# Kernel optimization log

Measured on AMD Instinct MI355X. Metric: run time of the kernel, lower is better.

Reference implementation:

```python
import jax, jax.numpy as jnp
import numpy as np

N, E, G = 100000, 1600000, 256      # nodes, edges, graphs in batch
IN_C, HID, OUT_C = 4, 128, 120
ALPHA = 0.5


def setup_inputs() -> dict:
    key = jax.random.key(0)
    ks = jax.random.split(key, 12)
    def w(k, i, o):
        return jax.random.normal(k, (i, o), jnp.float32) / np.float32(np.sqrt(i))
    return {
        "x": jax.random.normal(ks[0], (N, IN_C), jnp.float32),
        "edge_index": jax.random.randint(ks[1], (2, E), 0, N),
        "batch_seg": jnp.sort(jax.random.randint(ks[2], (N,), 0, G)),
        # DirGNNConv holds two independent GCNConvs (in / reversed direction)
        "W_in": w(ks[3], IN_C, HID),  "b_in": jnp.zeros((HID,), jnp.float32),
        "W_in_r": w(ks[4], IN_C, HID), "b_in_r": jnp.zeros((HID,), jnp.float32),
        "W_mid": w(ks[5], HID, HID),  "b_mid": jnp.zeros((HID,), jnp.float32),
        "W_mid_r": w(ks[6], HID, HID), "b_mid_r": jnp.zeros((HID,), jnp.float32),
        "W_out": w(ks[7], HID, OUT_C), "b_out": jnp.zeros((OUT_C,), jnp.float32),
        "W_out_r": w(ks[8], HID, OUT_C), "b_out_r": jnp.zeros((OUT_C,), jnp.float32),
    }


def _gcn(x, W, b, src, dst, n):
    # GCNConv with add_self_loops=False (DirGNNConv disables self-loops):
    # deg computed on destination side, norm = deg^-1/2[src] * deg^-1/2[dst]
    deg = jax.ops.segment_sum(jnp.ones(src.shape[0], x.dtype), dst, num_segments=n)
    dinv = jnp.where(deg > 0, jax.lax.rsqrt(jnp.maximum(deg, 1e-12)), 0.0)
    h = x @ W                                  # [N, out]
    msg = h[src] * (dinv[src] * dinv[dst])[:, None]  # gather + edge-normalize
    return jax.ops.segment_sum(msg, dst, num_segments=n) + b


def _dir_conv(x, Wi, bi, Wr, br, src, dst):
    # DirGNNConv(root_weight=False): (1-a)*conv(edge_index) + a*conv(flipped)
    n = x.shape[0]
    x_in = _gcn(x, Wi, bi, src, dst, n)
    x_out = _gcn(x, Wr, br, dst, src, n)
    return ALPHA * x_out + (1.0 - ALPHA) * x_in


def reference(x, edge_index, batch_seg, W_in, b_in, W_in_r, b_in_r,
              W_mid, b_mid, W_mid_r, b_mid_r, W_out, b_out, W_out_r, b_out_r):
    src, dst = edge_index[0], edge_index[1]
    h = jax.nn.relu(_dir_conv(x, W_in, b_in, W_in_r, b_in_r, src, dst))
    # dropout: eval mode -> identity
    h = jax.nn.relu(_dir_conv(h, W_mid, b_mid, W_mid_r, b_mid_r, src, dst))
    h = _dir_conv(h, W_out, b_out, W_out_r, b_out_r, src, dst)
    # global_mean_pool over batch_seg
    sums = jax.ops.segment_sum(h, batch_seg, num_segments=G)
    cnt = jax.ops.segment_sum(jnp.ones((h.shape[0],), h.dtype), batch_seg, num_segments=G)
    return sums / jnp.maximum(cnt, 1.0)[:, None]
```

## Files before the change

### kernel.cpp

```cpp
#include <hip/hip_runtime.h>
#include <hip/hip_fp16.h>

#define ALPHA 0.5f
#define SCAN_B 256
#define BSH 9
#define BSZ 512
#define MAXB 512
#define CHUNK 4096

static inline int ceil_div(int a, int b) { return (a + b - 1) / b; }

struct alignas(8) half4 { __half2 a, b; };

typedef _Float16 half8 __attribute__((ext_vector_type(8)));
typedef float f32x4 __attribute__((ext_vector_type(4)));

__global__ void hist_kernel(const int* __restrict__ src, const int* __restrict__ dst,
                            unsigned int* __restrict__ bhI, unsigned int* __restrict__ bhO,
                            int E, int nbuck)
{
    __shared__ unsigned int hI[MAXB], hO[MAXB];
    for (int b = threadIdx.x; b < MAXB; b += blockDim.x) { hI[b] = 0; hO[b] = 0; }
    __syncthreads();
    for (int e = blockIdx.x * blockDim.x + threadIdx.x; e < E; e += gridDim.x * blockDim.x) {
        atomicAdd(&hI[dst[e] >> BSH], 1u);
        atomicAdd(&hO[src[e] >> BSH], 1u);
    }
    __syncthreads();
    for (int b = threadIdx.x; b < nbuck; b += blockDim.x) {
        if (hI[b]) atomicAdd(&bhI[b], hI[b]);
        if (hO[b]) atomicAdd(&bhO[b], hO[b]);
    }
}

__global__ void bucket_base_kernel(const unsigned int* __restrict__ bhI,
                                   const unsigned int* __restrict__ bhO,
                                   unsigned int* __restrict__ baseI, unsigned int* __restrict__ baseO,
                                   unsigned int* __restrict__ curI, unsigned int* __restrict__ curO,
                                   int nbuck)
{
    __shared__ unsigned int tI[MAXB], tO[MAXB];
    int t = threadIdx.x;
    unsigned int vI = (t < nbuck) ? bhI[t] : 0u;
    unsigned int vO = (t < nbuck) ? bhO[t] : 0u;
    tI[t] = vI; tO[t] = vO;
    __syncthreads();
    for (int o = 1; o < MAXB; o <<= 1) {
        unsigned int xI = (t >= o) ? tI[t - o] : 0u;
        unsigned int xO = (t >= o) ? tO[t - o] : 0u;
        __syncthreads();
        tI[t] += xI; tO[t] += xO;
        __syncthreads();
    }
    if (t < nbuck) {
        baseI[t] = tI[t] - vI; baseO[t] = tO[t] - vO;
        curI[t]  = tI[t] - vI; curO[t]  = tO[t] - vO;
    }
}

__global__ void bucket_scatter_kernel(const int* __restrict__ src, const int* __restrict__ dst,
                                      unsigned int* __restrict__ curI, unsigned int* __restrict__ curO,
                                      int2* __restrict__ ebI, int2* __restrict__ ebO, int E)
{
    __shared__ unsigned int cI[MAXB], cO[MAXB], bI[MAXB], bO[MAXB];
    int t = threadIdx.x;
    for (int b = t; b < MAXB; b += blockDim.x) { cI[b] = 0; cO[b] = 0; }
    __syncthreads();
    int e0 = blockIdx.x * CHUNK;
    int e1 = min(E, e0 + CHUNK);
    for (int e = e0 + t; e < e1; e += blockDim.x) {
        atomicAdd(&cI[dst[e] >> BSH], 1u);
        atomicAdd(&cO[src[e] >> BSH], 1u);
    }
    __syncthreads();
    for (int b = t; b < MAXB; b += blockDim.x) {
        unsigned int n = cI[b];
        if (n) bI[b] = atomicAdd(&curI[b], n);
        cI[b] = 0;
        n = cO[b];
        if (n) bO[b] = atomicAdd(&curO[b], n);
        cO[b] = 0;
    }
    __syncthreads();
    for (int e = e0 + t; e < e1; e += blockDim.x) {
        int s = src[e], d = dst[e];
        int lb = d >> BSH;
        unsigned int p = bI[lb] + atomicAdd(&cI[lb], 1u);
        ebI[p] = make_int2(d, s);
        lb = s >> BSH;
        p = bO[lb] + atomicAdd(&cO[lb], 1u);
        ebO[p] = make_int2(s, d);
    }
}

__global__ void bucket_deg2_kernel(const int2* __restrict__ ebI, const int2* __restrict__ ebO,
                                   const unsigned int* __restrict__ baseI, const unsigned int* __restrict__ baseO,
                                   const unsigned int* __restrict__ bendI, const unsigned int* __restrict__ bendO,
                                   unsigned int* __restrict__ degI, unsigned int* __restrict__ degO, int N)
{
    const int2* __restrict__ eb          = blockIdx.y ? ebO : ebI;
    const unsigned int* __restrict__ base = blockIdx.y ? baseO : baseI;
    const unsigned int* __restrict__ bend = blockIdx.y ? bendO : bendI;
    unsigned int* __restrict__ deg        = blockIdx.y ? degO : degI;
    __shared__ unsigned int d[BSZ];
    int b = blockIdx.x, t = threadIdx.x;
    for (int i = t; i < BSZ; i += blockDim.x) d[i] = 0;
    __syncthreads();
    unsigned int lo = base[b], hi = bend[b];
    int nbase = b << BSH;
    for (unsigned int i = lo + t; i < hi; i += blockDim.x)
        atomicAdd(&d[eb[i].x - nbase], 1u);
    __syncthreads();
    for (int i = t; i < BSZ; i += blockDim.x) {
        int v = nbase + i;
        if (v < N) deg[v] = d[i];
    }
}

__global__ void bucket_adj2_kernel(const int2* __restrict__ ebI, const int2* __restrict__ ebO,
                                   const unsigned int* __restrict__ baseI, const unsigned int* __restrict__ baseO,
                                   const unsigned int* __restrict__ bendI, const unsigned int* __restrict__ bendO,
                                   const unsigned int* __restrict__ rowI, const unsigned int* __restrict__ rowO,
                                   int* __restrict__ adjI, int* __restrict__ adjO, int N)
{
    const int2* __restrict__ eb           = blockIdx.y ? ebO : ebI;
    const unsigned int* __restrict__ base  = blockIdx.y ? baseO : baseI;
    const unsigned int* __restrict__ bend  = blockIdx.y ? bendO : bendI;
    const unsigned int* __restrict__ rowst = blockIdx.y ? rowO : rowI;
    int* __restrict__ adj                  = blockIdx.y ? adjO : adjI;
    __shared__ unsigned int cur[BSZ];
    int b = blockIdx.x, t = threadIdx.x;
    int nbase = b << BSH;
    for (int i = t; i < BSZ; i += blockDim.x) {
        int v = nbase + i;
        cur[i] = (v < N) ? rowst[v] : 0u;
    }
    __syncthreads();
    unsigned int lo = base[b], hi = bend[b];
    for (unsigned int i = lo + t; i < hi; i += blockDim.x) {
        int2 e = eb[i];
        unsigned int p = atomicAdd(&cur[e.x - nbase], 1u);
        adj[p] = e.y;
    }
}

__global__ void scan_blk2_kernel(const unsigned int* __restrict__ degI, const unsigned int* __restrict__ degO,
                                 unsigned int* __restrict__ exclI, unsigned int* __restrict__ exclO,
                                 unsigned int* __restrict__ bsumI, unsigned int* __restrict__ bsumO, int N)
{
    const unsigned int* __restrict__ deg = blockIdx.y ? degO : degI;
    unsigned int* __restrict__ excl      = blockIdx.y ? exclO : exclI;
    unsigned int* __restrict__ bsum      = blockIdx.y ? bsumO : bsumI;
    __shared__ unsigned int tmp[SCAN_B];
    int t = threadIdx.x;
    int i = blockIdx.x * SCAN_B + t;
    unsigned int v = (i < N) ? deg[i] : 0u;
    tmp[t] = v;
    __syncthreads();
    for (int o = 1; o < SCAN_B; o <<= 1) {
        unsigned int x = (t >= o) ? tmp[t - o] : 0u;
        __syncthreads();
        tmp[t] += x;
        __syncthreads();
    }
    if (i < N) excl[i] = tmp[t] - v;
    if (t == SCAN_B - 1) bsum[blockIdx.x] = tmp[t];
}

__global__ void scan_top2_kernel(unsigned int* __restrict__ bsumI, unsigned int* __restrict__ bsumO, int nb)
{
    unsigned int* __restrict__ bsum = blockIdx.x ? bsumO : bsumI;
    __shared__ unsigned int tmp[1024];
    int t = threadIdx.x;
    unsigned int v = (t < nb) ? bsum[t] : 0u;
    tmp[t] = v;
    __syncthreads();
    for (int o = 1; o < 1024; o <<= 1) {
        unsigned int x = (t >= o) ? tmp[t - o] : 0u;
        __syncthreads();
        tmp[t] += x;
        __syncthreads();
    }
    if (t < nb) bsum[t] = tmp[t] - v;
}

__global__ void scan_add2_kernel(unsigned int* __restrict__ exclI, unsigned int* __restrict__ exclO,
                                 const unsigned int* __restrict__ bsumI, const unsigned int* __restrict__ bsumO,
                                 const unsigned int* __restrict__ degI, const unsigned int* __restrict__ degO,
                                 float* __restrict__ dinvI, float* __restrict__ dinvO, int N)
{
    unsigned int* __restrict__ excl       = blockIdx.y ? exclO : exclI;
    const unsigned int* __restrict__ bsum = blockIdx.y ? bsumO : bsumI;
    const unsigned int* __restrict__ deg  = blockIdx.y ? degO : degI;
    float* __restrict__ dinv              = blockIdx.y ? dinvO : dinvI;
    int i = blockIdx.x * SCAN_B + threadIdx.x;
    if (i < N) {
        excl[i] += bsum[blockIdx.x];
        unsigned int d = deg[i];
        dinv[i] = d ? rsqrtf((float)d) : 0.f;
    }
}

__global__ void seg_cnt_kernel(const int* __restrict__ seg, float* __restrict__ cnt, int N, int G)
{
    int g = blockIdx.x * blockDim.x + threadIdx.x;
    if (g >= G) return;
    int lo = 0, hi = N;
    while (lo < hi) { int m = (lo + hi) >> 1; if (seg[m] < g) lo = m + 1; else hi = m; }
    int s0 = lo;
    hi = N;
    while (lo < hi) { int m = (lo + hi) >> 1; if (seg[m] < g + 1) lo = m + 1; else hi = m; }
    cnt[g] = (float)(lo - s0);
}

__global__ void prep_w_kernel(const float* __restrict__ Wi, const float* __restrict__ Wr,
                              const float* __restrict__ bi, const float* __restrict__ br,
                              __half* __restrict__ Wt, float* __restrict__ bcomb)
{
    int idx = blockIdx.x * 256 + threadIdx.x;
    if (idx < 128 * 256) {
        int j = idx >> 8, k = idx & 255;
        float w = (k < 128) ? (1.f - ALPHA) * Wi[k * 128 + j]
                            : ALPHA * Wr[(k - 128) * 128 + j];
        Wt[idx] = __float2half_rn(w);
    }
    if (idx < 128) bcomb[idx] = (1.f - ALPHA) * bi[idx] + ALPHA * br[idx];
}

__global__ void gather4_kernel(const unsigned int* __restrict__ rowI,
                               const unsigned int* __restrict__ degI,
                               const int* __restrict__ adjI,
                               const float* __restrict__ dinvI,
                               const unsigned int* __restrict__ rowO,
                               const unsigned int* __restrict__ degO,
                               const int* __restrict__ adjO,
                               const float* __restrict__ dinvO,
                               const float4* __restrict__ x4,
                               float4* __restrict__ accI, float4* __restrict__ accO, int N)
{
    int v = blockIdx.x * blockDim.x + threadIdx.x;
    if (v >= N) return;
    {
        unsigned int k = rowI[v], end = k + degI[v];
        float4 acc = {0.f, 0.f, 0.f, 0.f};
        for (; k < end; ++k) {
            int s = adjI[k];
            float w = dinvI[s];
            float4 xv = x4[s];
            acc.x += w * xv.x; acc.y += w * xv.y; acc.z += w * xv.z; acc.w += w * xv.w;
        }
        float dv = dinvI[v];
        accI[v] = make_float4(dv * acc.x, dv * acc.y, dv * acc.z, dv * acc.w);
    }
    {
        unsigned int k = rowO[v], end = k + degO[v];
        float4 acc = {0.f, 0.f, 0.f, 0.f};
        for (; k < end; ++k) {
            int s = adjO[k];
            float w = dinvO[s];
            float4 xv = x4[s];
            acc.x += w * xv.x; acc.y += w * xv.y; acc.z += w * xv.z; acc.w += w * xv.w;
        }
        float dv = dinvO[v];
        accO[v] = make_float4(dv * acc.x, dv * acc.y, dv * acc.z, dv * acc.w);
    }
}

#define L1_NODES 32
__global__ void layer1_kernel(const float* __restrict__ accI, const float* __restrict__ accO,
                              const float* __restrict__ Wi, const float* __restrict__ bi,
                              const float* __restrict__ Wr, const float* __restrict__ br,
                              __half* __restrict__ h1, int N)
{
    __shared__ float wI[4][128], wO[4][128], bb[128];
    int j = threadIdx.x;
    for (int c = 0; c < 4; ++c) {
        wI[c][j] = (1.f - ALPHA) * Wi[c * 128 + j];
        wO[c][j] = ALPHA * Wr[c * 128 + j];
    }
    bb[j] = (1.f - ALPHA) * bi[j] + ALPHA * br[j];
    __syncthreads();
    int v0 = blockIdx.x * L1_NODES;
    int v1 = min(N, v0 + L1_NODES);
    for (int v = v0; v < v1; ++v) {
        float s = bb[j];
#pragma unroll
        for (int c = 0; c < 4; ++c)
            s += accI[v * 4 + c] * wI[c][j] + accO[v * 4 + c] * wO[c][j];
        h1[(size_t)v * 128 + j] = __float2half_rn(fmaxf(s, 0.f));
    }
}

__global__ void gather128_kernel(const unsigned int* __restrict__ rowstartI,
                                 const unsigned int* __restrict__ degI,
                                 const int* __restrict__ adjI,
                                 const float* __restrict__ dinvI,
                                 const unsigned int* __restrict__ rowstartO,
                                 const unsigned int* __restrict__ degO,
                                 const int* __restrict__ adjO,
                                 const float* __restrict__ dinvO,
                                 const half8* __restrict__ hp,
                                 half8* __restrict__ outI, half8* __restrict__ outO, int N)
{
    int v = blockIdx.x * 16 + (threadIdx.x >> 4);
    if (v >= N) return;
    int lane = threadIdx.x & 15;
    const unsigned int* __restrict__ rowstart = blockIdx.y ? rowstartO : rowstartI;
    const unsigned int* __restrict__ deg      = blockIdx.y ? degO : degI;
    const int* __restrict__ adj               = blockIdx.y ? adjO : adjI;
    const float* __restrict__ dinv            = blockIdx.y ? dinvO : dinvI;
    half8* __restrict__ out                   = blockIdx.y ? outO : outI;

    unsigned int k = rowstart[v];
    unsigned int end = k + deg[v];
    float acc[8];
#pragma unroll
    for (int i = 0; i < 8; ++i) acc[i] = 0.f;

    for (; k + 2 <= end; k += 2) {
        int s0 = adj[k], s1 = adj[k + 1];
        float w0 = dinv[s0], w1 = dinv[s1];
        half8 h0 = hp[(size_t)s0 * 16 + lane];
        half8 h1 = hp[(size_t)s1 * 16 + lane];
#pragma unroll
        for (int i = 0; i < 8; ++i)
            acc[i] += w0 * (float)h0[i] + w1 * (float)h1[i];
    }
    if (k < end) {
        int s = adj[k];
        float w = dinv[s];
        half8 hv = hp[(size_t)s * 16 + lane];
#pragma unroll
        for (int i = 0; i < 8; ++i)
            acc[i] += w * (float)hv[i];
    }
    float dv = dinv[v];
    half8 o;
#pragma unroll
    for (int i = 0; i < 8; ++i) o[i] = (_Float16)(dv * acc[i]);
    out[(size_t)v * 16 + lane] = o;
}

__global__ __launch_bounds__(256) void layer2_mfma_kernel(
    const __half* __restrict__ aggI, const __half* __restrict__ aggO,
    const __half* __restrict__ Wt,
    const float* __restrict__ bcomb,
    __half* __restrict__ h2, int N)
{
    int wave = threadIdx.x >> 6;
    int lane = threadIdx.x & 63;
    int v0 = blockIdx.x * 64 + wave * 16;
    int row = lane & 15;
    int kg  = lane >> 4;
    int vsafe = min(v0 + row, N - 1);

    f32x4 acc[8];
#pragma unroll
    for (int t = 0; t < 8; ++t) acc[t] = (f32x4){0.f, 0.f, 0.f, 0.f};

#pragma unroll
    for (int ks = 0; ks < 8; ++ks) {
        const __half* asrc = (ks < 4) ? aggI : aggO;
        int kofs = (ks & 3) * 32 + kg * 8;
        half8 afrag = *(const half8*)&asrc[(size_t)vsafe * 128 + kofs];
        int kw = ks * 32 + kg * 8;
#pragma unroll
        for (int t = 0; t < 8; ++t) {
            int j = t * 16 + row;
            half8 bfrag = *(const half8*)&Wt[(size_t)j * 256 + kw];
            acc[t] = __builtin_amdgcn_mfma_f32_16x16x32_f16(afrag, bfrag, acc[t], 0, 0, 0);
        }
    }

#pragma unroll
    for (int t = 0; t < 8; ++t) {
        int j = t * 16 + row;
        float bj = bcomb[j];
#pragma unroll
        for (int r = 0; r < 4; ++r) {
            int vr = v0 + kg * 4 + r;
            if (vr < N)
                h2[(size_t)vr * 128 + j] = __float2half_rn(fmaxf(acc[t][r] + bj, 0.f));
        }
    }
}

#define POOL_NODES 32
__global__ void pool_kernel(const __half* __restrict__ aI, const __half* __restrict__ aO,
                            const int* __restrict__ seg,
                            float* __restrict__ poolI, float* __restrict__ poolO, int N)
{
    int j = threadIdx.x;
    int v0 = blockIdx.x * POOL_NODES;
    if (v0 >= N) return;
    int v1 = min(N, v0 + POOL_NODES);
    float sI = 0.f, sO = 0.f;
    int cur = seg[v0];
    for (int v = v0; v < v1; ++v) {
        int g = seg[v];
        if (g != cur) {
            atomicAdd(&poolI[cur * 128 + j], sI);
            atomicAdd(&poolO[cur * 128 + j], sO);
            sI = 0.f; sO = 0.f; cur = g;
        }
        sI += __half2float(aI[(size_t)v * 128 + j]);
        sO += __half2float(aO[(size_t)v * 128 + j]);
    }
    atomicAdd(&poolI[cur * 128 + j], sI);
    atomicAdd(&poolO[cur * 128 + j], sO);
}

__global__ void final_kernel(const float* __restrict__ poolI, const float* __restrict__ poolO,
                             const float* __restrict__ cnt,
                             const float* __restrict__ Wo, const float* __restrict__ bo,
                             const float* __restrict__ Wor, const float* __restrict__ bor,
                             float* __restrict__ out, int G)
{
    int g = blockIdx.x;
    int j = threadIdx.x;
    if (g >= G || j >= 120) return;
    float acc = 0.f;
    for (int k = 0; k < 128; ++k) {
        acc += poolI[g * 128 + k] * ((1.f - ALPHA) * Wo[k * 120 + j])
             + poolO[g * 128 + k] * (ALPHA * Wor[k * 120 + j]);
    }
    float c = cnt[g];
    float bcomb = (1.f - ALPHA) * bo[j] + ALPHA * bor[j];
    out[g * 120 + j] = (c > 0.f) ? (acc / c + bcomb) : 0.f;
}

extern "C" void kernel_launch(void* const* d_in, const int* in_sizes, int n_in,
                              void* d_out, int out_size, void* d_ws, size_t ws_size,
                              hipStream_t stream)
{
    const float* x      = (const float*)d_in[0];
    const int*   ei     = (const int*)d_in[1];
    const int*   seg    = (const int*)d_in[2];
    const float* W_in   = (const float*)d_in[3];
    const float* b_in   = (const float*)d_in[4];
    const float* W_in_r = (const float*)d_in[5];
    const float* b_in_r = (const float*)d_in[6];
    const float* W_mid  = (const float*)d_in[7];
    const float* b_mid  = (const float*)d_in[8];
    const float* W_mid_r= (const float*)d_in[9];
    const float* b_mid_r= (const float*)d_in[10];
    const float* W_out  = (const float*)d_in[11];
    const float* b_out  = (const float*)d_in[12];
    const float* W_out_r= (const float*)d_in[13];
    const float* b_out_r= (const float*)d_in[14];

    const int N = in_sizes[0] / 4;
    const int E = in_sizes[1] / 2;
    const int G = out_size / 120;
    const int* src = ei;
    const int* dst = ei + E;
    const int NBLK  = ceil_div(N, SCAN_B);
    const int NBUCK = ceil_div(N, BSZ);

    char* wsb = (char*)d_ws;
    size_t off = 0;
    auto alloc = [&](size_t elems) { void* p = wsb + off * 4; off += elems; return p; };

    unsigned int* bhI   = (unsigned int*)alloc(MAXB);
    unsigned int* bhO   = (unsigned int*)alloc(MAXB);
    float*        poolI = (float*)alloc((size_t)G * 128);
    float*        poolO = (float*)alloc((size_t)G * 128);
    size_t zero_elems = off;
    float*        cnt   = (float*)alloc(G);
    unsigned int* baseI = (unsigned int*)alloc(MAXB);
    unsigned int* baseO = (unsigned int*)alloc(MAXB);
    unsigned int* curI  = (unsigned int*)alloc(MAXB);
    unsigned int* curO  = (unsigned int*)alloc(MAXB);
    unsigned int* degI  = (unsigned int*)alloc(N);
    unsigned int* degO  = (unsigned int*)alloc(N);
    float*        dinvI = (float*)alloc(N);
    float*        dinvO = (float*)alloc(N);
    unsigned int* rowI  = (unsigned int*)alloc(N);
    unsigned int* rowO  = (unsigned int*)alloc(N);
    int*          adjI  = (int*)alloc(E);
    int*          adjO  = (int*)alloc(E);
    unsigned int* bsumI = (unsigned int*)alloc(1024);
    unsigned int* bsumO = (unsigned int*)alloc(1024);
    __half*       Wt    = (__half*)alloc(128 * 256 / 2);
    float*        bcomb = (float*)alloc(128);
    off = (off + 3) & ~(size_t)3;
    float* acc4I = (float*)alloc((size_t)N * 4);
    float* acc4O = (float*)alloc((size_t)N * 4);
    __half* hbuf = (__half*)alloc((size_t)N * 64);
    __half* aggI = (__half*)alloc((size_t)N * 64);
    __half* aggO = (__half*)alloc((size_t)N * 64);
    (void)ws_size;

    int2* ebI = (int2*)aggI;
    int2* ebO = (int2*)aggO;

    hipMemsetAsync(d_ws, 0, zero_elems * 4, stream);

    const int T = 256;
    hist_kernel<<<ceil_div(E, T * 16), T, 0, stream>>>(src, dst, bhI, bhO, E, NBUCK);
    bucket_base_kernel<<<1, MAXB, 0, stream>>>(bhI, bhO, baseI, baseO, curI, curO, NBUCK);
    bucket_scatter_kernel<<<ceil_div(E, CHUNK), T, 0, stream>>>(src, dst, curI, curO, ebI, ebO, E);
    bucket_deg2_kernel<<<dim3(NBUCK, 2), T, 0, stream>>>(ebI, ebO, baseI, baseO, curI, curO,
                                                         degI, degO, N);
    scan_blk2_kernel<<<dim3(NBLK, 2), SCAN_B, 0, stream>>>(degI, degO, rowI, rowO, bsumI, bsumO, N);
    scan_top2_kernel<<<2, 1024, 0, stream>>>(bsumI, bsumO, NBLK);
    scan_add2_kernel<<<dim3(NBLK, 2), SCAN_B, 0, stream>>>(rowI, rowO, bsumI, bsumO,
                                                           degI, degO, dinvI, dinvO, N);
    bucket_adj2_kernel<<<dim3(NBUCK, 2), T, 0, stream>>>(ebI, ebO, baseI, baseO, curI, curO,
                                                         rowI, rowO, adjI, adjO, N);
    seg_cnt_kernel<<<ceil_div(G, T), T, 0, stream>>>(seg, cnt, N, G);
    prep_w_kernel<<<128, 256, 0, stream>>>(W_mid, W_mid_r, b_mid, b_mid_r, Wt, bcomb);

    gather4_kernel<<<ceil_div(N, T), T, 0, stream>>>(rowI, degI, adjI, dinvI,
                                                     rowO, degO, adjO, dinvO,
                                                     (const float4*)x,
                                                     (float4*)acc4I, (float4*)acc4O, N);
    layer1_kernel<<<ceil_div(N, L1_NODES), 128, 0, stream>>>(acc4I, acc4O,
                                                             W_in, b_in, W_in_r, b_in_r, hbuf, N);
    gather128_kernel<<<dim3(ceil_div(N, 16), 2), 256, 0, stream>>>(
        rowI, degI, adjI, dinvI, rowO, degO, adjO, dinvO,
        (const half8*)hbuf, (half8*)aggI, (half8*)aggO, N);
    layer2_mfma_kernel<<<ceil_div(N, 64), 256, 0, stream>>>(
        aggI, aggO, Wt, bcomb, hbuf, N);
    gather128_kernel<<<dim3(ceil_div(N, 16), 2), 256, 0, stream>>>(
        rowI, degI, adjI, dinvI, rowO, degO, adjO, dinvO,
        (const half8*)hbuf, (half8*)aggI, (half8*)aggO, N);
    pool_kernel<<<ceil_div(N, POOL_NODES), 128, 0, stream>>>(
        aggI, aggO, seg, poolI, poolO, N);
    final_kernel<<<G, 128, 0, stream>>>(poolI, poolO, cnt,
                                        W_out, b_out, W_out_r, b_out_r, (float*)d_out, G);
}
```

Before: 509.5 us.

## Fuse CSR build into one bucket kernel, fuse layer-1 gather+GEMV, unroll gather

Merges the bucket degree count, the three-stage global scan, and the adjacency fill into a single per-bucket kernel. It computes row offsets from the bucket base plus a local shared-memory scan, which removes four launches and the round trips of deg/row through global memory. Layer 1 now aggregates the 4-channel input and applies the 4x128 weights in the same thread, so the intermediate accumulator buffers disappear. The 128-wide gather loop is unrolled by 4 to keep more loads in flight. One risk is the fused layer-1 kernel, where each thread writes 256 bytes with strided per-thread stores.

```diff
diff --git a/kernel.cpp b/kernel.cpp
--- a/kernel.cpp
+++ b/kernel.cpp
@@ -2,15 +2,12 @@
 #include <hip/hip_fp16.h>
 
 #define ALPHA 0.5f
-#define SCAN_B 256
 #define BSH 9
 #define BSZ 512
 #define MAXB 512
 #define CHUNK 4096
 
 static inline int ceil_div(int a, int b) { return (a + b - 1) / b; }
-
-struct alignas(8) half4 { __half2 a, b; };
 
 typedef _Float16 half8 __attribute__((ext_vector_type(8)));
 typedef float f32x4 __attribute__((ext_vector_type(4)));
@@ -93,111 +90,65 @@
     }
 }
 
-__global__ void bucket_deg2_kernel(const int2* __restrict__ ebI, const int2* __restrict__ ebO,
-                                   const unsigned int* __restrict__ baseI, const unsigned int* __restrict__ baseO,
-                                   const unsigned int* __restrict__ bendI, const unsigned int* __restrict__ bendO,
-                                   unsigned int* __restrict__ degI, unsigned int* __restrict__ degO, int N)
-{
-    const int2* __restrict__ eb          = blockIdx.y ? ebO : ebI;
+__global__ __launch_bounds__(256) void bucket_csr_kernel(
+    const int2* __restrict__ ebI, const int2* __restrict__ ebO,
+    const unsigned int* __restrict__ baseI, const unsigned int* __restrict__ baseO,
+    const unsigned int* __restrict__ bendI, const unsigned int* __restrict__ bendO,
+    unsigned int* __restrict__ rowI, unsigned int* __restrict__ rowO,
+    unsigned int* __restrict__ degI, unsigned int* __restrict__ degO,
+    float* __restrict__ dinvI, float* __restrict__ dinvO,
+    int* __restrict__ adjI, int* __restrict__ adjO, int N)
+{
+    const int2* __restrict__ eb           = blockIdx.y ? ebO : ebI;
     const unsigned int* __restrict__ base = blockIdx.y ? baseO : baseI;
     const unsigned int* __restrict__ bend = blockIdx.y ? bendO : bendI;
+    unsigned int* __restrict__ row        = blockIdx.y ? rowO : rowI;
     unsigned int* __restrict__ deg        = blockIdx.y ? degO : degI;
+    float* __restrict__ dinv              = blockIdx.y ? dinvO : dinvI;
+    int* __restrict__ adj                 = blockIdx.y ? adjO : adjI;
+
     __shared__ unsigned int d[BSZ];
-    int b = blockIdx.x, t = threadIdx.x;
-    for (int i = t; i < BSZ; i += blockDim.x) d[i] = 0;
-    __syncthreads();
-    unsigned int lo = base[b], hi = bend[b];
-    int nbase = b << BSH;
-    for (unsigned int i = lo + t; i < hi; i += blockDim.x)
-        atomicAdd(&d[eb[i].x - nbase], 1u);
-    __syncthreads();
-    for (int i = t; i < BSZ; i += blockDim.x) {
-        int v = nbase + i;
-        if (v < N) deg[v] = d[i];
-    }
-}
-
-__global__ void bucket_adj2_kernel(const int2* __restrict__ ebI, const int2* __restrict__ ebO,
-                                   const unsigned int* __restrict__ baseI, const unsigned int* __restrict__ baseO,
-                                   const unsigned int* __restrict__ bendI, const unsigned int* __restrict__ bendO,
-                                   const unsigned int* __restrict__ rowI, const unsigned int* __restrict__ rowO,
-                                   int* __restrict__ adjI, int* __restrict__ adjO, int N)
-{
-    const int2* __restrict__ eb           = blockIdx.y ? ebO : ebI;
-    const unsigned int* __restrict__ base  = blockIdx.y ? baseO : baseI;
-    const unsigned int* __restrict__ bend  = blockIdx.y ? bendO : bendI;
-    const unsigned int* __restrict__ rowst = blockIdx.y ? rowO : rowI;
-    int* __restrict__ adj                  = blockIdx.y ? adjO : adjI;
-    __shared__ unsigned int cur[BSZ];
+    __shared__ unsigned int ex[BSZ];
+    __shared__ unsigned int ps[256];
     int b = blockIdx.x, t = threadIdx.x;
     int nbase = b << BSH;
-    for (int i = t; i < BSZ; i += blockDim.x) {
+
+    for (int i = t; i < BSZ; i += 256) d[i] = 0;
+    __syncthreads();
+    unsigned int lo = base[b], hi = bend[b];
+    for (unsigned int i = lo + t; i < hi; i += 256)
+        atomicAdd(&d[eb[i].x - nbase], 1u);
+    __syncthreads();
+
+    ps[t] = d[2 * t] + d[2 * t + 1];
+    __syncthreads();
+    for (int o = 1; o < 256; o <<= 1) {
+        unsigned int x = (t >= o) ? ps[t - o] : 0u;
+        __syncthreads();
+        ps[t] += x;
+        __syncthreads();
+    }
+    unsigned int p0 = (t > 0) ? ps[t - 1] : 0u;
+    ex[2 * t]     = p0;
+    ex[2 * t + 1] = p0 + d[2 * t];
+    __syncthreads();
+
+    for (int i = t; i < BSZ; i += 256) {
         int v = nbase + i;
-        cur[i] = (v < N) ? rowst[v] : 0u;
-    }
-    __syncthreads();
-    unsigned int lo = base[b], hi = bend[b];
-    for (unsigned int i = lo + t; i < hi; i += blockDim.x) {
+        if (v < N) {
+            unsigned int dd = d[i];
+            row[v]  = lo + ex[i];
+            deg[v]  = dd;
+            dinv[v] = dd ? rsqrtf((float)dd) : 0.f;
+        }
+    }
+    __syncthreads();
+    for (int i = t; i < BSZ; i += 256) d[i] = lo + ex[i];
+    __syncthreads();
+    for (unsigned int i = lo + t; i < hi; i += 256) {
         int2 e = eb[i];
-        unsigned int p = atomicAdd(&cur[e.x - nbase], 1u);
+        unsigned int p = atomicAdd(&d[e.x - nbase], 1u);
         adj[p] = e.y;
-    }
-}
-
-__global__ void scan_blk2_kernel(const unsigned int* __restrict__ degI, const unsigned int* __restrict__ degO,
-                                 unsigned int* __restrict__ exclI, unsigned int* __restrict__ exclO,
-                                 unsigned int* __restrict__ bsumI, unsigned int* __restrict__ bsumO, int N)
-{
-    const unsigned int* __restrict__ deg = blockIdx.y ? degO : degI;
-    unsigned int* __restrict__ excl      = blockIdx.y ? exclO : exclI;
-    unsigned int* __restrict__ bsum      = blockIdx.y ? bsumO : bsumI;
-    __shared__ unsigned int tmp[SCAN_B];
-    int t = threadIdx.x;
-    int i = blockIdx.x * SCAN_B + t;
-    unsigned int v = (i < N) ? deg[i] : 0u;
-    tmp[t] = v;
-    __syncthreads();
-    for (int o = 1; o < SCAN_B; o <<= 1) {
-        unsigned int x = (t >= o) ? tmp[t - o] : 0u;
-        __syncthreads();
-        tmp[t] += x;
-        __syncthreads();
-    }
-    if (i < N) excl[i] = tmp[t] - v;
-    if (t == SCAN_B - 1) bsum[blockIdx.x] = tmp[t];
-}
-
-__global__ void scan_top2_kernel(unsigned int* __restrict__ bsumI, unsigned int* __restrict__ bsumO, int nb)
-{
-    unsigned int* __restrict__ bsum = blockIdx.x ? bsumO : bsumI;
-    __shared__ unsigned int tmp[1024];
-    int t = threadIdx.x;
-    unsigned int v = (t < nb) ? bsum[t] : 0u;
-    tmp[t] = v;
-    __syncthreads();
-    for (int o = 1; o < 1024; o <<= 1) {
-        unsigned int x = (t >= o) ? tmp[t - o] : 0u;
-        __syncthreads();
-        tmp[t] += x;
-        __syncthreads();
-    }
-    if (t < nb) bsum[t] = tmp[t] - v;
-}
-
-__global__ void scan_add2_kernel(unsigned int* __restrict__ exclI, unsigned int* __restrict__ exclO,
-                                 const unsigned int* __restrict__ bsumI, const unsigned int* __restrict__ bsumO,
-                                 const unsigned int* __restrict__ degI, const unsigned int* __restrict__ degO,
-                                 float* __restrict__ dinvI, float* __restrict__ dinvO, int N)
-{
-    unsigned int* __restrict__ excl       = blockIdx.y ? exclO : exclI;
-    const unsigned int* __restrict__ bsum = blockIdx.y ? bsumO : bsumI;
-    const unsigned int* __restrict__ deg  = blockIdx.y ? degO : degI;
-    float* __restrict__ dinv              = blockIdx.y ? dinvO : dinvI;
-    int i = blockIdx.x * SCAN_B + threadIdx.x;
-    if (i < N) {
-        excl[i] += bsum[blockIdx.x];
-        unsigned int d = deg[i];
-        dinv[i] = d ? rsqrtf((float)d) : 0.f;
     }
 }
 
@@ -227,67 +178,68 @@
     if (idx < 128) bcomb[idx] = (1.f - ALPHA) * bi[idx] + ALPHA * br[idx];
 }
 
-__global__ void gather4_kernel(const unsigned int* __restrict__ rowI,
-                               const unsigned int* __restrict__ degI,
-                               const int* __restrict__ adjI,
-                               const float* __restrict__ dinvI,
-                               const unsigned int* __restrict__ rowO,
-                               const unsigned int* __restrict__ degO,
-                               const int* __restrict__ adjO,
-                               const float* __restrict__ dinvO,
-                               const float4* __restrict__ x4,
-                               float4* __restrict__ accI, float4* __restrict__ accO, int N)
-{
-    int v = blockIdx.x * blockDim.x + threadIdx.x;
+__global__ __launch_bounds__(256) void layer1_fused_kernel(
+    const unsigned int* __restrict__ rowI, const unsigned int* __restrict__ degI,
+    const int* __restrict__ adjI, const float* __restrict__ dinvI,
+    const unsigned int* __restrict__ rowO, const unsigned int* __restrict__ degO,
+    const int* __restrict__ adjO, const float* __restrict__ dinvO,
+    const float4* __restrict__ x4,
+    const float* __restrict__ Wi, const float* __restrict__ bi,
+    const float* __restrict__ Wr, const float* __restrict__ br,
+    __half* __restrict__ h1, int N)
+{
+    __shared__ float wI[4][128], wO[4][128], bb[128];
+    int t = threadIdx.x;
+    if (t < 128) {
+#pragma unroll
+        for (int c = 0; c < 4; ++c) {
+            wI[c][t] = (1.f - ALPHA) * Wi[c * 128 + t];
+            wO[c][t] = ALPHA * Wr[c * 128 + t];
+        }
+        bb[t] = (1.f - ALPHA) * bi[t] + ALPHA * br[t];
+    }
+    __syncthreads();
+    int v = blockIdx.x * 256 + t;
     if (v >= N) return;
+
+    float4 aI = {0.f, 0.f, 0.f, 0.f};
     {
         unsigned int k = rowI[v], end = k + degI[v];
-        float4 acc = {0.f, 0.f, 0.f, 0.f};
         for (; k < end; ++k) {
             int s = adjI[k];
             float w = dinvI[s];
             float4 xv = x4[s];
-            acc.x += w * xv.x; acc.y += w * xv.y; acc.z += w * xv.z; acc.w += w * xv.w;
+            aI.x += w * xv.x; aI.y += w * xv.y; aI.z += w * xv.z; aI.w += w * xv.w;
         }
         float dv = dinvI[v];
-        accI[v] = make_float4(dv * acc.x, dv * acc.y, dv * acc.z, dv * acc.w);
-    }
+        aI.x *= dv; aI.y *= dv; aI.z *= dv; aI.w *= dv;
+    }
+    float4 aO = {0.f, 0.f, 0.f, 0.f};
     {
         unsigned int k = rowO[v], end = k + degO[v];
-        float4 acc = {0.f, 0.f, 0.f, 0.f};
         for (; k < end; ++k) {
             int s = adjO[k];
             float w = dinvO[s];
             float4 xv = x4[s];
-            acc.x += w * xv.x; acc.y += w * xv.y; acc.z += w * xv.z; acc.w += w * xv.w;
+            aO.x += w * xv.x; aO.y += w * xv.y; aO.z += w * xv.z; aO.w += w * xv.w;
         }
         float dv = dinvO[v];
-        accO[v] = make_float4(dv * acc.x, dv * acc.y, dv * acc.z, dv * acc.w);
-    }
-}
-
-#define L1_NODES 32
-__global__ void layer1_kernel(const float* __restrict__ accI, const float* __restrict__ accO,
-                              const float* __restrict__ Wi, const float* __restrict__ bi,
-                              const float* __restrict__ Wr, const float* __restrict__ br,
-                              __half* __restrict__ h1, int N)
-{
-    __shared__ float wI[4][128], wO[4][128], bb[128];
-    int j = threadIdx.x;
-    for (int c = 0; c < 4; ++c) {
-        wI[c][j] = (1.f - ALPHA) * Wi[c * 128 + j];
-        wO[c][j] = ALPHA * Wr[c * 128 + j];
-    }
-    bb[j] = (1.f - ALPHA) * bi[j] + ALPHA * br[j];
-    __syncthreads();
-    int v0 = blockIdx.x * L1_NODES;
-    int v1 = min(N, v0 + L1_NODES);
-    for (int v = v0; v < v1; ++v) {
-        float s = bb[j];
-#pragma unroll
-        for (int c = 0; c < 4; ++c)
-            s += accI[v * 4 + c] * wI[c][j] + accO[v * 4 + c] * wO[c][j];
-        h1[(size_t)v * 128 + j] = __float2half_rn(fmaxf(s, 0.f));
+        aO.x *= dv; aO.y *= dv; aO.z *= dv; aO.w *= dv;
+    }
+
+    half8* outp = (half8*)&h1[(size_t)v * 128];
+#pragma unroll
+    for (int jq = 0; jq < 16; ++jq) {
+        half8 o;
+#pragma unroll
+        for (int u = 0; u < 8; ++u) {
+            int j = jq * 8 + u;
+            float s = bb[j]
+                    + aI.x * wI[0][j] + aI.y * wI[1][j] + aI.z * wI[2][j] + aI.w * wI[3][j]
+                    + aO.x * wO[0][j] + aO.y * wO[1][j] + aO.z * wO[2][j] + aO.w * wO[3][j];
+            o[u] = (_Float16)fmaxf(s, 0.f);
+        }
+        outp[jq] = o;
     }
 }
 
@@ -317,16 +269,19 @@
 #pragma unroll
     for (int i = 0; i < 8; ++i) acc[i] = 0.f;
 
-    for (; k + 2 <= end; k += 2) {
-        int s0 = adj[k], s1 = adj[k + 1];
-        float w0 = dinv[s0], w1 = dinv[s1];
+    for (; k + 4 <= end; k += 4) {
+        int s0 = adj[k], s1 = adj[k + 1], s2 = adj[k + 2], s3 = adj[k + 3];
+        float w0 = dinv[s0], w1 = dinv[s1], w2 = dinv[s2], w3 = dinv[s3];
         half8 h0 = hp[(size_t)s0 * 16 + lane];
         half8 h1 = hp[(size_t)s1 * 16 + lane];
+        half8 h2 = hp[(size_t)s2 * 16 + lane];
+        half8 h3 = hp[(size_t)s3 * 16 + lane];
 #pragma unroll
         for (int i = 0; i < 8; ++i)
-            acc[i] += w0 * (float)h0[i] + w1 * (float)h1[i];
-    }
-    if (k < end) {
+            acc[i] += w0 * (float)h0[i] + w1 * (float)h1[i]
+                    + w2 * (float)h2[i] + w3 * (float)h3[i];
+    }
+    for (; k < end; ++k) {
         int s = adj[k];
         float w = dinv[s];
         half8 hv = hp[(size_t)s * 16 + lane];
@@ -454,7 +409,6 @@
     const int G = out_size / 120;
     const int* src = ei;
     const int* dst = ei + E;
-    const int NBLK  = ceil_div(N, SCAN_B);
     const int NBUCK = ceil_div(N, BSZ);
 
     char* wsb = (char*)d_ws;
@@ -479,13 +433,9 @@
     unsigned int* rowO  = (unsigned int*)alloc(N);
     int*          adjI  = (int*)alloc(E);
     int*          adjO  = (int*)alloc(E);
-    unsigned int* bsumI = (unsigned int*)alloc(1024);
-    unsigned int* bsumO = (unsigned int*)alloc(1024);
     __half*       Wt    = (__half*)alloc(128 * 256 / 2);
     float*        bcomb = (float*)alloc(128);
     off = (off + 3) & ~(size_t)3;
-    float* acc4I = (float*)alloc((size_t)N * 4);
-    float* acc4O = (float*)alloc((size_t)N * 4);
     __half* hbuf = (__half*)alloc((size_t)N * 64);
     __half* aggI = (__half*)alloc((size_t)N * 64);
     __half* aggO = (__half*)alloc((size_t)N * 64);
@@ -500,23 +450,15 @@
     hist_kernel<<<ceil_div(E, T * 16), T, 0, stream>>>(src, dst, bhI, bhO, E, NBUCK);
     bucket_base_kernel<<<1, MAXB, 0, stream>>>(bhI, bhO, baseI, baseO, curI, curO, NBUCK);
     bucket_scatter_kernel<<<ceil_div(E, CHUNK), T, 0, stream>>>(src, dst, curI, curO, ebI, ebO, E);
-    bucket_deg2_kernel<<<dim3(NBUCK, 2), T, 0, stream>>>(ebI, ebO, baseI, baseO, curI, curO,
-                                                         degI, degO, N);
-    scan_blk2_kernel<<<dim3(NBLK, 2), SCAN_B, 0, stream>>>(degI, degO, rowI, rowO, bsumI, bsumO, N);
-    scan_top2_kernel<<<2, 1024, 0, stream>>>(bsumI, bsumO, NBLK);
-    scan_add2_kernel<<<dim3(NBLK, 2), SCAN_B, 0, stream>>>(rowI, rowO, bsumI, bsumO,
-                                                           degI, degO, dinvI, dinvO, N);
-    bucket_adj2_kernel<<<dim3(NBUCK, 2), T, 0, stream>>>(ebI, ebO, baseI, baseO, curI, curO,
-                                                         rowI, rowO, adjI, adjO, N);
+    bucket_csr_kernel<<<dim3(NBUCK, 2), T, 0, stream>>>(ebI, ebO, baseI, baseO, curI, curO,
+                                                        rowI, rowO, degI, degO,
+                                                        dinvI, dinvO, adjI, adjO, N);
     seg_cnt_kernel<<<ceil_div(G, T), T, 0, stream>>>(seg, cnt, N, G);
     prep_w_kernel<<<128, 256, 0, stream>>>(W_mid, W_mid_r, b_mid, b_mid_r, Wt, bcomb);
 
-    gather4_kernel<<<ceil_div(N, T), T, 0, stream>>>(rowI, degI, adjI, dinvI,
-                                                     rowO, degO, adjO, dinvO,
-                                                     (const float4*)x,
-                                                     (float4*)acc4I, (float4*)acc4O, N);
-    layer1_kernel<<<ceil_div(N, L1_NODES), 128, 0, stream>>>(acc4I, acc4O,
-                                                             W_in, b_in, W_in_r, b_in_r, hbuf, N);
+    layer1_fused_kernel<<<ceil_div(N, T), T, 0, stream>>>(
+        rowI, degI, adjI, dinvI, rowO, degO, adjO, dinvO,
+        (const float4*)x, W_in, b_in, W_in_r, b_in_r, hbuf, N);
     gather128_kernel<<<dim3(ceil_div(N, 16), 2), 256, 0, stream>>>(
         rowI, degI, adjI, dinvI, rowO, degO, adjO, dinvO,
         (const half8*)hbuf, (half8*)aggI, (half8*)aggO, N);
```

After: 480.4 us. 1.06x faster.
